# Kernel optimization log

Measured on AMD Instinct MI355X. Metric: run time of the kernel, lower is better.

Reference implementation:

```python
import jax, jax.numpy as jnp
import numpy as np

NUM_FEAT = 512
NUM_HEAD = 8
DEPTH = NUM_FEAT // NUM_HEAD
B, S = 2, 4096


def setup_inputs() -> dict:
    key = jax.random.key(0)
    ks = jax.random.split(key, 12)
    sc = 1.0 / np.sqrt(NUM_FEAT)
    inp = {
        "q": jax.random.normal(ks[0], (B, S, NUM_FEAT), jnp.float32),
        "k": jax.random.normal(ks[1], (B, S, NUM_FEAT), jnp.float32),
        "v": jax.random.normal(ks[2], (B, S, NUM_FEAT), jnp.float32),
        # causal mask: 1 where attention is disallowed (upper triangle), additive style
        "mask": jnp.triu(jnp.ones((S, S), jnp.float32), k=1)[None, None, :, :],
        "wq": jax.random.normal(ks[3], (NUM_FEAT, NUM_FEAT), jnp.float32) * sc,
        "bq": jnp.zeros((NUM_FEAT,), jnp.float32),
        "wk": jax.random.normal(ks[4], (NUM_FEAT, NUM_FEAT), jnp.float32) * sc,
        "bk": jnp.zeros((NUM_FEAT,), jnp.float32),
        "wv": jax.random.normal(ks[5], (NUM_FEAT, NUM_FEAT), jnp.float32) * sc,
        "bv": jnp.zeros((NUM_FEAT,), jnp.float32),
        "wo": jax.random.normal(ks[6], (NUM_FEAT, NUM_FEAT), jnp.float32) * sc,
        "bo": jnp.zeros((NUM_FEAT,), jnp.float32),
    }
    return inp


def _split_heads(x):
    b, s, _ = x.shape
    return x.reshape(b, s, NUM_HEAD, DEPTH).transpose(0, 2, 1, 3)  # [B,H,S,D]


def reference(q, k, v, mask, wq, bq, wk, bk, wv, bv, wo, bo):
    qh = _split_heads(q @ wq + bq)
    kh = _split_heads(k @ wk + bk)
    vh = _split_heads(v @ wv + bv)
    # scaled dot-product attention with materialized [B,H,S,S] scores
    logits = jnp.einsum("bhqd,bhkd->bhqk", qh, kh) / jnp.sqrt(jnp.float32(DEPTH))
    logits = logits + mask * (-1e9)
    weights = jax.nn.softmax(logits, axis=-1)
    attn = jnp.einsum("bhqk,bhkd->bhqd", weights, vh)
    concat = attn.transpose(0, 2, 1, 3).reshape(q.shape[0], -1, NUM_FEAT)
    return concat @ wo + bo
```

## Files before the change

### kernel.cpp

```cpp
#include <hip/hip_runtime.h>
#include <hip/hip_bf16.h>
#include <stdint.h>

#define NB 2
#define NS 4096
#define NF 512
#define NH 8
#define ND 64
#define NM (NB * NS)

typedef __attribute__((ext_vector_type(8))) short bf16x8;
typedef __attribute__((ext_vector_type(4))) float f32x4;
typedef __attribute__((ext_vector_type(16))) float f32x16;

static __device__ __forceinline__ unsigned short f2bf(float f) {
    union { float f; uint32_t u; } x; x.f = f;
    uint32_t u = x.u;
    u += 0x7FFFu + ((u >> 16) & 1u);
    return (unsigned short)(u >> 16);
}

static __device__ __forceinline__ void load_lds16(const void* g, void* l) {
    __builtin_amdgcn_global_load_lds(
        (const __attribute__((address_space(1))) void*)g,
        (__attribute__((address_space(3))) void*)l,
        16, 0, 0);
}

__global__ void convert_all(const float* __restrict__ q, const float* __restrict__ k,
                            const float* __restrict__ v,
                            unsigned short* __restrict__ qb, unsigned short* __restrict__ kb,
                            unsigned short* __restrict__ vb,
                            const float* __restrict__ wq, const float* __restrict__ wk,
                            const float* __restrict__ wv, const float* __restrict__ wo,
                            unsigned short* __restrict__ o0, unsigned short* __restrict__ o1,
                            unsigned short* __restrict__ o2, unsigned short* __restrict__ o3) {
    int i0 = blockIdx.x * blockDim.x + threadIdx.x;
    int stride = gridDim.x * blockDim.x;
    const int n4 = (NB * NS * NF) / 4;
    for (int i = i0; i < n4; i += stride) {
        float4 a = ((const float4*)q)[i];
        float4 b = ((const float4*)k)[i];
        float4 c = ((const float4*)v)[i];
        ushort4 oa, ob, oc;
        oa.x = f2bf(a.x); oa.y = f2bf(a.y); oa.z = f2bf(a.z); oa.w = f2bf(a.w);
        ob.x = f2bf(b.x); ob.y = f2bf(b.y); ob.z = f2bf(b.z); ob.w = f2bf(b.w);
        oc.x = f2bf(c.x); oc.y = f2bf(c.y); oc.z = f2bf(c.z); oc.w = f2bf(c.w);
        ((ushort4*)qb)[i] = oa;
        ((ushort4*)kb)[i] = ob;
        ((ushort4*)vb)[i] = oc;
    }
    for (int i = i0; i < 4 * NF * NF; i += stride) {
        int w = i >> 18;
        int off = i & (NF * NF - 1);
        int r = off >> 9;
        int c = off & (NF - 1);
        const float* src = (w == 0) ? wq : (w == 1) ? wk : (w == 2) ? wv : wo;
        unsigned short* dst = (w == 0) ? o0 : (w == 1) ? o1 : (w == 2) ? o2 : o3;
        dst[c * NF + r] = f2bf(src[off]);
    }
}

__launch_bounds__(256, 2)
__global__ void proj_qkv(const unsigned short* __restrict__ Aq,
                         const unsigned short* __restrict__ Ak,
                         const unsigned short* __restrict__ Av,
                         const unsigned short* __restrict__ WqT,
                         const unsigned short* __restrict__ WkT,
                         const unsigned short* __restrict__ WvT,
                         const float* __restrict__ bq, const float* __restrict__ bk,
                         const float* __restrict__ bv,
                         unsigned short* __restrict__ Qh, unsigned short* __restrict__ Kh,
                         unsigned short* __restrict__ VTs) {
    __shared__ char smem[65536];

    const int mode = blockIdx.z;
    const unsigned short* A  = (mode == 0) ? Aq : (mode == 1) ? Ak : Av;
    const unsigned short* WT = (mode == 0) ? WqT : (mode == 1) ? WkT : WvT;
    const float* bias        = (mode == 0) ? bq : (mode == 1) ? bk : bv;

    const int t = threadIdx.x;
    const int wid = t >> 6;
    const int lane = t & 63;
    const int l15 = lane & 15;
    const int lhi = lane >> 4;
    const int m0 = blockIdx.x * 128;
    const int n0 = blockIdx.y * 128;
    const int wm = (wid >> 1) * 64;
    const int wn = (wid & 1) * 64;

    const int srow = t >> 3;
    const int scol = ((t & 7) * 16) ^ ((srow & 7) << 4);

    const f32x4 zero4 = {0.f, 0.f, 0.f, 0.f};
    f32x4 acc[4][4];
#pragma unroll
    for (int i = 0; i < 4; ++i)
#pragma unroll
        for (int j = 0; j < 4; ++j) acc[i][j] = zero4;

    auto STAGE = [&](int buf, int k0) {
        char* As = smem + buf * 32768;
        char* Bs = As + 16384;
#pragma unroll
        for (int i = 0; i < 4; ++i) {
            const char* sa = (const char*)A + ((size_t)(m0 + i * 32 + srow) * NF + k0) * 2 + scol;
            load_lds16(sa, As + i * 4096 + wid * 1024);
            const char* sb = (const char*)WT + ((size_t)(n0 + i * 32 + srow) * NF + k0) * 2 + scol;
            load_lds16(sb, Bs + i * 4096 + wid * 1024);
        }
    };

    STAGE(0, 0);
    int cur = 0;
    for (int kt = 0; kt < 8; ++kt) {
        if (kt < 7) {
            STAGE(cur ^ 1, (kt + 1) * 64);
            asm volatile("s_waitcnt vmcnt(8)" ::: "memory");
        } else {
            asm volatile("s_waitcnt vmcnt(0)" ::: "memory");
        }
        __builtin_amdgcn_s_barrier();
        __builtin_amdgcn_sched_barrier(0);

        const char* As = smem + cur * 32768;
        const char* Bs = As + 16384;
#pragma unroll
        for (int ks = 0; ks < 2; ++ks) {
            bf16x8 af[4], bfr[4];
#pragma unroll
            for (int i = 0; i < 4; ++i) {
                int ra = wm + i * 16 + l15;
                int ca = (ks * 64 + lhi * 16) ^ ((ra & 7) << 4);
                af[i] = *(const bf16x8*)(As + ra * 128 + ca);
                int rb = wn + i * 16 + l15;
                int cb = (ks * 64 + lhi * 16) ^ ((rb & 7) << 4);
                bfr[i] = *(const bf16x8*)(Bs + rb * 128 + cb);
            }
#pragma unroll
            for (int mi = 0; mi < 4; ++mi)
#pragma unroll
                for (int ni = 0; ni < 4; ++ni)
                    acc[mi][ni] = __builtin_amdgcn_mfma_f32_16x16x32_bf16(af[mi], bfr[ni], acc[mi][ni], 0, 0, 0);
        }
        __builtin_amdgcn_sched_barrier(0);
        __builtin_amdgcn_s_barrier();
        cur ^= 1;
    }

#pragma unroll
    for (int ni = 0; ni < 4; ++ni) {
        int col = n0 + wn + ni * 16 + l15;
        float bv2 = bias[col];
#pragma unroll
        for (int mi = 0; mi < 4; ++mi) {
#pragma unroll
            for (int r = 0; r < 4; ++r) {
                int row = m0 + wm + mi * 16 + lhi * 4 + r;
                float val = acc[mi][ni][r] + bv2;
                int b = row >> 12, s = row & (NS - 1);
                int hh = col >> 6, d = col & (ND - 1);
                if (mode == 0) {
                    val *= 0.125f;
                    Qh[((size_t)(b * NH + hh) * NS + s) * ND + d] = f2bf(val);
                } else if (mode == 1) {
                    Kh[((size_t)(b * NH + hh) * NS + s) * ND + d] = f2bf(val);
                } else {
                    VTs[((size_t)(b * NH + hh) * ND + d) * NS + s] = f2bf(val);
                }
            }
        }
    }
}

__launch_bounds__(256, 2)
__global__ void proj_o(const unsigned short* __restrict__ A,
                       const unsigned short* __restrict__ WT,
                       const float* __restrict__ bias,
                       float* __restrict__ Out) {
    __shared__ char smem[49152];

    const int t = threadIdx.x;
    const int wid = t >> 6;
    const int lane = t & 63;
    const int l15 = lane & 15;
    const int lhi = lane >> 4;
    const int m0 = blockIdx.x * 64;
    const int n0 = blockIdx.y * 128;
    const int wm = (wid >> 1) * 32;
    const int wn = (wid & 1) * 64;

    const int srow = t >> 3;
    const int scol = ((t & 7) * 16) ^ ((srow & 7) << 4);

    const f32x4 zero4 = {0.f, 0.f, 0.f, 0.f};
    f32x4 acc[2][4];
#pragma unroll
    for (int i = 0; i < 2; ++i)
#pragma unroll
        for (int j = 0; j < 4; ++j) acc[i][j] = zero4;

    auto STAGE = [&](int buf, int k0) {
        char* As = smem + buf * 24576;
        char* Bs = As + 8192;
#pragma unroll
        for (int i = 0; i < 2; ++i) {
            const char* sa = (const char*)A + ((size_t)(m0 + i * 32 + srow) * NF + k0) * 2 + scol;
            load_lds16(sa, As + i * 4096 + wid * 1024);
        }
#pragma unroll
        for (int i = 0; i < 4; ++i) {
            const char* sb = (const char*)WT + ((size_t)(n0 + i * 32 + srow) * NF + k0) * 2 + scol;
            load_lds16(sb, Bs + i * 4096 + wid * 1024);
        }
    };

    STAGE(0, 0);
    int cur = 0;
    for (int kt = 0; kt < 8; ++kt) {
        if (kt < 7) {
            STAGE(cur ^ 1, (kt + 1) * 64);
            asm volatile("s_waitcnt vmcnt(6)" ::: "memory");
        } else {
            asm volatile("s_waitcnt vmcnt(0)" ::: "memory");
        }
        __builtin_amdgcn_s_barrier();
        __builtin_amdgcn_sched_barrier(0);

        const char* As = smem + cur * 24576;
        const char* Bs = As + 8192;
#pragma unroll
        for (int ks = 0; ks < 2; ++ks) {
            bf16x8 af[2], bfr[4];
#pragma unroll
            for (int i = 0; i < 2; ++i) {
                int ra = wm + i * 16 + l15;
                int ca = (ks * 64 + lhi * 16) ^ ((ra & 7) << 4);
                af[i] = *(const bf16x8*)(As + ra * 128 + ca);
            }
#pragma unroll
            for (int i = 0; i < 4; ++i) {
                int rb = wn + i * 16 + l15;
                int cb = (ks * 64 + lhi * 16) ^ ((rb & 7) << 4);
                bfr[i] = *(const bf16x8*)(Bs + rb * 128 + cb);
            }
#pragma unroll
            for (int mi = 0; mi < 2; ++mi)
#pragma unroll
                for (int ni = 0; ni < 4; ++ni)
                    acc[mi][ni] = __builtin_amdgcn_mfma_f32_16x16x32_bf16(af[mi], bfr[ni], acc[mi][ni], 0, 0, 0);
        }
        __builtin_amdgcn_sched_barrier(0);
        __builtin_amdgcn_s_barrier();
        cur ^= 1;
    }

#pragma unroll
    for (int ni = 0; ni < 4; ++ni) {
        int col = n0 + wn + ni * 16 + l15;
        float bv2 = bias[col];
#pragma unroll
        for (int mi = 0; mi < 2; ++mi)
#pragma unroll
            for (int r = 0; r < 4; ++r) {
                int row = m0 + wm + mi * 16 + lhi * 4 + r;
                Out[(size_t)row * NF + col] = acc[mi][ni][r] + bv2;
            }
    }
}

__launch_bounds__(256, 2)
__global__ void attn_fused(const unsigned short* __restrict__ Qh,
                           const unsigned short* __restrict__ Kh,
                           const unsigned short* __restrict__ VT,
                           unsigned short* __restrict__ Cc) {
    __shared__ char smem[65536];

    const int t = threadIdx.x;
    const int wid = t >> 6;
    const int pair = wid >> 1;
    const int a = wid & 1;
    const int lane = t & 63;
    const int l31 = lane & 31;
    const int h = lane >> 5;
    const int qt = 63 - (int)blockIdx.x;
    const int hh = blockIdx.y, b = blockIdx.z;
    const int q0 = qt * 64;
    const size_t bh = (size_t)b * NH + hh;
    const char* Qp = (const char*)(Qh + bh * NS * ND);
    const char* Kp = (const char*)(Kh + bh * NS * ND);
    const char* Vp = (const char*)(VT + bh * (size_t)ND * NS);

    const int qrow = q0 + a * 32 + l31;
    bf16x8 qf[4];
#pragma unroll
    for (int kc = 0; kc < 4; ++kc)
        qf[kc] = *(const bf16x8*)(Qp + (size_t)qrow * 128 + kc * 32 + h * 16);

    f32x16 o[2];
#pragma unroll
    for (int r = 0; r < 16; ++r) { o[0][r] = 0.f; o[1][r] = 0.f; }
    float m_run = -1e30f, l_run = 0.f;

    const int srow = lane >> 3;
    const int scol = ((lane & 7) * 16) ^ ((srow & 7) << 4);
    const size_t koff = (size_t)srow * 128 + scol;
    const size_t voff = (size_t)srow * (NS * 2) + scol;
    char* pbase = smem + pair * 32768;

    auto STAGE = [&](int buf, int kv0) {
        char* dst = pbase + buf * 16384;
        if (a == 0) {
            const char* g = Kp + (size_t)kv0 * 128 + koff;
#pragma unroll
            for (int i = 0; i < 8; ++i)
                load_lds16(g + i * 1024, dst + i * 1024);
        } else {
            const char* g = Vp + (size_t)kv0 * 2 + voff;
            char* lv = dst + 8192;
#pragma unroll
            for (int i = 0; i < 8; ++i)
                load_lds16(g + (size_t)i * 8 * (NS * 2), lv + i * 1024);
        }
    };

    const int myC = (qt + 2 - pair) >> 1;
    const int R = (qt + 2) >> 1;
    const int sw = (l31 & 7) << 4;

    if (0 < myC) STAGE(0, pair * 64);
    int cur = 0;

    for (int j = 0; j < R; ++j) {
        if (j + 1 < myC) {
            STAGE(cur ^ 1, (2 * (j + 1) + pair) * 64);
            asm volatile("s_waitcnt vmcnt(8)" ::: "memory");
        } else {
            asm volatile("s_waitcnt vmcnt(0)" ::: "memory");
        }
        __builtin_amdgcn_s_barrier();
        __builtin_amdgcn_sched_barrier(0);

        if (j < myC) {
            const int kt = 2 * j + pair;
            const char* Kb = pbase + cur * 16384;
            const char* Vb = Kb + 8192;

            f32x16 sT[2];
#pragma unroll
            for (int r = 0; r < 16; ++r) { sT[0][r] = 0.f; sT[1][r] = 0.f; }
#pragma unroll
            for (int kvi = 0; kvi < 2; ++kvi) {
                const int row = kvi * 32 + l31;
#pragma unroll
                for (int kc = 0; kc < 4; ++kc) {
                    bf16x8 kf = *(const bf16x8*)(Kb + row * 128 + ((kc * 32 + h * 16) ^ sw));
                    sT[kvi] = __builtin_amdgcn_mfma_f32_32x32x16_bf16(kf, qf[kc], sT[kvi], 0, 0, 0);
                }
            }

            if (kt == qt) {
#pragma unroll
                for (int kvi = 0; kvi < 2; ++kvi)
#pragma unroll
                    for (int r = 0; r < 16; ++r) {
                        int kv = kt * 64 + kvi * 32 + (r & 3) + ((r >> 2) << 3) + h * 4;
                        if (kv > qrow) sT[kvi][r] = -1e30f;
                    }
            }

            float pm = -1e30f;
#pragma unroll
            for (int kvi = 0; kvi < 2; ++kvi)
#pragma unroll
                for (int r = 0; r < 16; ++r) pm = fmaxf(pm, sT[kvi][r]);
            pm = fmaxf(pm, __shfl_xor(pm, 32));

            if (__ballot(pm > m_run + 8.0f) != 0ull) {
                float mnew = fmaxf(m_run, pm);
                float sc = __expf(m_run - mnew);
                m_run = mnew;
                l_run *= sc;
#pragma unroll
                for (int di = 0; di < 2; ++di)
#pragma unroll
                    for (int r = 0; r < 16; ++r) o[di][r] *= sc;
            }
            float rs = 0.f;
#pragma unroll
            for (int kvi = 0; kvi < 2; ++kvi)
#pragma unroll
                for (int r = 0; r < 16; ++r) {
                    float p = __expf(sT[kvi][r] - m_run);
                    sT[kvi][r] = p;
                    rs += p;
                }
            rs += __shfl_xor(rs, 32);
            l_run += rs;

            unsigned int w[2][8];
#pragma unroll
            for (int kvi = 0; kvi < 2; ++kvi)
#pragma unroll
                for (int i = 0; i < 8; ++i)
                    w[kvi][i] = (unsigned int)f2bf(sT[kvi][2 * i]) |
                                ((unsigned int)f2bf(sT[kvi][2 * i + 1]) << 16);

            union FB { unsigned int u[4]; bf16x8 v; };
            bf16x8 pf[4];
#pragma unroll
            for (int ck = 0; ck < 4; ++ck) {
                const int kvi = ck >> 1, pb = (ck & 1) * 4;
                unsigned int aSrc = h ? w[kvi][pb + 0] : w[kvi][pb + 2];
                unsigned int bSrc = h ? w[kvi][pb + 1] : w[kvi][pb + 3];
                unsigned int sA = (unsigned int)__shfl_xor((int)aSrc, 32);
                unsigned int sB = (unsigned int)__shfl_xor((int)bSrc, 32);
                FB f;
                f.u[0] = (h == 0) ? w[kvi][pb + 0] : sA;
                f.u[1] = (h == 0) ? w[kvi][pb + 1] : sB;
                f.u[2] = (h == 0) ? sA : w[kvi][pb + 2];
                f.u[3] = (h == 0) ? sB : w[kvi][pb + 3];
                pf[ck] = f.v;
            }

#pragma unroll
            for (int di = 0; di < 2; ++di) {
                const int row = di * 32 + l31;
#pragma unroll
                for (int ck = 0; ck < 4; ++ck) {
                    bf16x8 vf = *(const bf16x8*)(Vb + row * 128 + ((ck * 32 + h * 16) ^ sw));
                    o[di] = __builtin_amdgcn_mfma_f32_32x32x16_bf16(vf, pf[ck], o[di], 0, 0, 0);
                }
            }
        }

        __builtin_amdgcn_sched_barrier(0);
        __builtin_amdgcn_s_barrier();
        cur ^= 1;
    }

    __syncthreads();
    float* xch = (float*)smem;
    const int xi = (a * 64 + lane) * 34;
    if (pair == 1) {
        xch[xi] = m_run;
        xch[xi + 1] = l_run;
#pragma unroll
        for (int di = 0; di < 2; ++di)
#pragma unroll
            for (int r = 0; r < 16; ++r) xch[xi + 2 + di * 16 + r] = o[di][r];
    }
    __syncthreads();
    if (pair == 0) {
        float m1 = xch[xi], l1 = xch[xi + 1];
        float m = fmaxf(m_run, m1);
        float e0 = __expf(m_run - m);
        float e1 = __expf(m1 - m);
        float inv = 1.f / (l_run * e0 + l1 * e1);
        size_t obase = ((size_t)b * NS + qrow) * NF + hh * ND;
#pragma unroll
        for (int di = 0; di < 2; ++di)
#pragma unroll
            for (int tq = 0; tq < 4; ++tq) {
                ushort4 pk;
                pk.x = f2bf((o[di][4 * tq + 0] * e0 + xch[xi + 2 + di * 16 + 4 * tq + 0] * e1) * inv);
                pk.y = f2bf((o[di][4 * tq + 1] * e0 + xch[xi + 2 + di * 16 + 4 * tq + 1] * e1) * inv);
                pk.z = f2bf((o[di][4 * tq + 2] * e0 + xch[xi + 2 + di * 16 + 4 * tq + 2] * e1) * inv);
                pk.w = f2bf((o[di][4 * tq + 3] * e0 + xch[xi + 2 + di * 16 + 4 * tq + 3] * e1) * inv);
                *(ushort4*)(Cc + obase + di * 32 + tq * 8 + h * 4) = pk;
            }
    }
}

extern "C" void kernel_launch(void* const* d_in, const int* in_sizes, int n_in,
                              void* d_out, int out_size, void* d_ws, size_t ws_size,
                              hipStream_t stream) {
    const float* q = (const float*)d_in[0];
    const float* k = (const float*)d_in[1];
    const float* v = (const float*)d_in[2];
    const float* wq = (const float*)d_in[4];
    const float* bq = (const float*)d_in[5];
    const float* wk = (const float*)d_in[6];
    const float* bk = (const float*)d_in[7];
    const float* wv = (const float*)d_in[8];
    const float* bv = (const float*)d_in[9];
    const float* wo = (const float*)d_in[10];
    const float* bo = (const float*)d_in[11];

    const size_t MB = 1u << 20;
    char* ws = (char*)d_ws;
    unsigned short* qb  = (unsigned short*)(ws);
    unsigned short* kb  = (unsigned short*)(ws + 8 * MB);
    unsigned short* vb  = (unsigned short*)(ws + 16 * MB);
    unsigned short* wqT = (unsigned short*)(ws + 24 * MB);
    unsigned short* wkT = (unsigned short*)(ws + 24 * MB + 512 * 1024);
    unsigned short* wvT = (unsigned short*)(ws + 25 * MB);
    unsigned short* woT = (unsigned short*)(ws + 25 * MB + 512 * 1024);
    unsigned short* Qh  = (unsigned short*)(ws + 26 * MB);
    unsigned short* Kh  = (unsigned short*)(ws + 34 * MB);
    unsigned short* VTs = (unsigned short*)(ws + 42 * MB);

    convert_all<<<dim3(2048), dim3(256), 0, stream>>>(q, k, v, qb, kb, vb,
                                                      wq, wk, wv, wo, wqT, wkT, wvT, woT);

    proj_qkv<<<dim3(NM / 128, NF / 128, 3), dim3(256), 0, stream>>>(
        qb, kb, vb, wqT, wkT, wvT, bq, bk, bv, Qh, Kh, VTs);

    attn_fused<<<dim3(64, NH, NB), dim3(256), 0, stream>>>(Qh, Kh, VTs, qb );

    proj_o<<<dim3(NM / 64, NF / 128), dim3(256), 0, stream>>>(qb, woT, bo, (float*)d_out);
}
```

Baseline: 319.3 us.

## Restructure attention to single-wave blocks loading K/V directly into registers

Replaces the 4-wave block, which split the KV range between two wave pairs sharing LDS double buffers and then merged their softmax states, with one 64-thread block per 32-query tile. Each wave now walks the full causal KV range and ping-pongs K fragments in registers, loading them straight from global memory with no LDS, barriers or cross-pair merge. The grid grows to 2048 single-wave blocks ordered longest-first. This removes LDS staging and sync overhead but gives up K/V reuse across waves, so every wave reads K and V from global or cache on its own and register pressure rises.

```diff
diff --git a/kernel.cpp b/kernel.cpp
--- a/kernel.cpp
+++ b/kernel.cpp
@@ -269,29 +269,24 @@
     }
 }
 
-__launch_bounds__(256, 2)
+__launch_bounds__(64, 2)
 __global__ void attn_fused(const unsigned short* __restrict__ Qh,
                            const unsigned short* __restrict__ Kh,
                            const unsigned short* __restrict__ VT,
                            unsigned short* __restrict__ Cc) {
-    __shared__ char smem[65536];
-
-    const int t = threadIdx.x;
-    const int wid = t >> 6;
-    const int pair = wid >> 1;
-    const int a = wid & 1;
-    const int lane = t & 63;
+    const int lane = threadIdx.x;
     const int l31 = lane & 31;
     const int h = lane >> 5;
-    const int qt = 63 - (int)blockIdx.x;
-    const int hh = blockIdx.y, b = blockIdx.z;
-    const int q0 = qt * 64;
-    const size_t bh = (size_t)b * NH + hh;
-    const char* Qp = (const char*)(Qh + bh * NS * ND);
-    const char* Kp = (const char*)(Kh + bh * NS * ND);
-    const char* Vp = (const char*)(VT + bh * (size_t)ND * NS);
-
-    const int qrow = q0 + a * 32 + l31;
+    const int k = blockIdx.x;
+    const int bh = k & 15;
+    const int g = 127 - (k >> 4);
+    const int b = bh >> 3, hh = bh & 7;
+    const size_t bhs = (size_t)b * NH + hh;
+    const char* Qp = (const char*)(Qh + bhs * NS * ND);
+    const char* Kp = (const char*)(Kh + bhs * NS * ND);
+    const char* Vp = (const char*)(VT + bhs * (size_t)ND * NS);
+
+    const int qrow = g * 32 + l31;
     bf16x8 qf[4];
 #pragma unroll
     for (int kc = 0; kc < 4; ++kc)
@@ -302,174 +297,133 @@
     for (int r = 0; r < 16; ++r) { o[0][r] = 0.f; o[1][r] = 0.f; }
     float m_run = -1e30f, l_run = 0.f;
 
-    const int srow = lane >> 3;
-    const int scol = ((lane & 7) * 16) ^ ((srow & 7) << 4);
-    const size_t koff = (size_t)srow * 128 + scol;
-    const size_t voff = (size_t)srow * (NS * 2) + scol;
-    char* pbase = smem + pair * 32768;
-
-    auto STAGE = [&](int buf, int kv0) {
-        char* dst = pbase + buf * 16384;
-        if (a == 0) {
-            const char* g = Kp + (size_t)kv0 * 128 + koff;
+    const int nkv = (g >> 1) + 1;
+
+    auto LOADK = [&](int t, bf16x8* kf) {
+        const char* base = Kp + (size_t)t * 64 * 128;
+#pragma unroll
+        for (int kvi = 0; kvi < 2; ++kvi)
+#pragma unroll
+            for (int kc = 0; kc < 4; ++kc)
+                kf[kvi * 4 + kc] = *(const bf16x8*)(base + (kvi * 32 + l31) * 128 + kc * 32 + h * 16);
+    };
+    auto LOADV = [&](int t, bf16x8* vf) {
+        const char* base = Vp + (size_t)t * 128;
+#pragma unroll
+        for (int di = 0; di < 2; ++di)
+#pragma unroll
+            for (int ck = 0; ck < 4; ++ck)
+                vf[di * 4 + ck] = *(const bf16x8*)(base + (size_t)(di * 32 + l31) * (NS * 2) + ck * 32 + h * 16);
+    };
+
+    auto TILE = [&](int t, const bf16x8* kf, const bf16x8* vf) {
+        f32x16 sT[2];
+#pragma unroll
+        for (int r = 0; r < 16; ++r) { sT[0][r] = 0.f; sT[1][r] = 0.f; }
+#pragma unroll
+        for (int kvi = 0; kvi < 2; ++kvi)
+#pragma unroll
+            for (int kc = 0; kc < 4; ++kc)
+                sT[kvi] = __builtin_amdgcn_mfma_f32_32x32x16_bf16(kf[kvi * 4 + kc], qf[kc], sT[kvi], 0, 0, 0);
+
+        if (t == nkv - 1) {
+#pragma unroll
+            for (int kvi = 0; kvi < 2; ++kvi)
+#pragma unroll
+                for (int r = 0; r < 16; ++r) {
+                    int kv = t * 64 + kvi * 32 + (r & 3) + ((r >> 2) << 3) + h * 4;
+                    if (kv > qrow) sT[kvi][r] = -1e30f;
+                }
+        }
+
+        float pm = -1e30f;
+#pragma unroll
+        for (int kvi = 0; kvi < 2; ++kvi)
+#pragma unroll
+            for (int r = 0; r < 16; ++r) pm = fmaxf(pm, sT[kvi][r]);
+        pm = fmaxf(pm, __shfl_xor(pm, 32));
+
+        if (__ballot(pm > m_run + 8.0f) != 0ull) {
+            float mnew = fmaxf(m_run, pm);
+            float sc = __expf(m_run - mnew);
+            m_run = mnew;
+            l_run *= sc;
+#pragma unroll
+            for (int di = 0; di < 2; ++di)
+#pragma unroll
+                for (int r = 0; r < 16; ++r) o[di][r] *= sc;
+        }
+        float rs = 0.f;
+#pragma unroll
+        for (int kvi = 0; kvi < 2; ++kvi)
+#pragma unroll
+            for (int r = 0; r < 16; ++r) {
+                float p = __expf(sT[kvi][r] - m_run);
+                sT[kvi][r] = p;
+                rs += p;
+            }
+        rs += __shfl_xor(rs, 32);
+        l_run += rs;
+
+        unsigned int w[2][8];
+#pragma unroll
+        for (int kvi = 0; kvi < 2; ++kvi)
 #pragma unroll
             for (int i = 0; i < 8; ++i)
-                load_lds16(g + i * 1024, dst + i * 1024);
-        } else {
-            const char* g = Vp + (size_t)kv0 * 2 + voff;
-            char* lv = dst + 8192;
-#pragma unroll
-            for (int i = 0; i < 8; ++i)
-                load_lds16(g + (size_t)i * 8 * (NS * 2), lv + i * 1024);
-        }
+                w[kvi][i] = (unsigned int)f2bf(sT[kvi][2 * i]) |
+                            ((unsigned int)f2bf(sT[kvi][2 * i + 1]) << 16);
+
+        union FB { unsigned int u[4]; bf16x8 v; };
+        bf16x8 pf[4];
+#pragma unroll
+        for (int ck = 0; ck < 4; ++ck) {
+            const int kvi = ck >> 1, pb = (ck & 1) * 4;
+            unsigned int aSrc = h ? w[kvi][pb + 0] : w[kvi][pb + 2];
+            unsigned int bSrc = h ? w[kvi][pb + 1] : w[kvi][pb + 3];
+            unsigned int sA = (unsigned int)__shfl_xor((int)aSrc, 32);
+            unsigned int sB = (unsigned int)__shfl_xor((int)bSrc, 32);
+            FB f;
+            f.u[0] = (h == 0) ? w[kvi][pb + 0] : sA;
+            f.u[1] = (h == 0) ? w[kvi][pb + 1] : sB;
+            f.u[2] = (h == 0) ? sA : w[kvi][pb + 2];
+            f.u[3] = (h == 0) ? sB : w[kvi][pb + 3];
+            pf[ck] = f.v;
+        }
+
+#pragma unroll
+        for (int di = 0; di < 2; ++di)
+#pragma unroll
+            for (int ck = 0; ck < 4; ++ck)
+                o[di] = __builtin_amdgcn_mfma_f32_32x32x16_bf16(vf[di * 4 + ck], pf[ck], o[di], 0, 0, 0);
     };
 
-    const int myC = (qt + 2 - pair) >> 1;
-    const int R = (qt + 2) >> 1;
-    const int sw = (l31 & 7) << 4;
-
-    if (0 < myC) STAGE(0, pair * 64);
-    int cur = 0;
-
-    for (int j = 0; j < R; ++j) {
-        if (j + 1 < myC) {
-            STAGE(cur ^ 1, (2 * (j + 1) + pair) * 64);
-            asm volatile("s_waitcnt vmcnt(8)" ::: "memory");
-        } else {
-            asm volatile("s_waitcnt vmcnt(0)" ::: "memory");
-        }
-        __builtin_amdgcn_s_barrier();
-        __builtin_amdgcn_sched_barrier(0);
-
-        if (j < myC) {
-            const int kt = 2 * j + pair;
-            const char* Kb = pbase + cur * 16384;
-            const char* Vb = Kb + 8192;
-
-            f32x16 sT[2];
-#pragma unroll
-            for (int r = 0; r < 16; ++r) { sT[0][r] = 0.f; sT[1][r] = 0.f; }
-#pragma unroll
-            for (int kvi = 0; kvi < 2; ++kvi) {
-                const int row = kvi * 32 + l31;
-#pragma unroll
-                for (int kc = 0; kc < 4; ++kc) {
-                    bf16x8 kf = *(const bf16x8*)(Kb + row * 128 + ((kc * 32 + h * 16) ^ sw));
-                    sT[kvi] = __builtin_amdgcn_mfma_f32_32x32x16_bf16(kf, qf[kc], sT[kvi], 0, 0, 0);
-                }
-            }
-
-            if (kt == qt) {
-#pragma unroll
-                for (int kvi = 0; kvi < 2; ++kvi)
-#pragma unroll
-                    for (int r = 0; r < 16; ++r) {
-                        int kv = kt * 64 + kvi * 32 + (r & 3) + ((r >> 2) << 3) + h * 4;
-                        if (kv > qrow) sT[kvi][r] = -1e30f;
-                    }
-            }
-
-            float pm = -1e30f;
-#pragma unroll
-            for (int kvi = 0; kvi < 2; ++kvi)
-#pragma unroll
-                for (int r = 0; r < 16; ++r) pm = fmaxf(pm, sT[kvi][r]);
-            pm = fmaxf(pm, __shfl_xor(pm, 32));
-
-            if (__ballot(pm > m_run + 8.0f) != 0ull) {
-                float mnew = fmaxf(m_run, pm);
-                float sc = __expf(m_run - mnew);
-                m_run = mnew;
-                l_run *= sc;
-#pragma unroll
-                for (int di = 0; di < 2; ++di)
-#pragma unroll
-                    for (int r = 0; r < 16; ++r) o[di][r] *= sc;
-            }
-            float rs = 0.f;
-#pragma unroll
-            for (int kvi = 0; kvi < 2; ++kvi)
-#pragma unroll
-                for (int r = 0; r < 16; ++r) {
-                    float p = __expf(sT[kvi][r] - m_run);
-                    sT[kvi][r] = p;
-                    rs += p;
-                }
-            rs += __shfl_xor(rs, 32);
-            l_run += rs;
-
-            unsigned int w[2][8];
-#pragma unroll
-            for (int kvi = 0; kvi < 2; ++kvi)
-#pragma unroll
-                for (int i = 0; i < 8; ++i)
-                    w[kvi][i] = (unsigned int)f2bf(sT[kvi][2 * i]) |
-                                ((unsigned int)f2bf(sT[kvi][2 * i + 1]) << 16);
-
-            union FB { unsigned int u[4]; bf16x8 v; };
-            bf16x8 pf[4];
-#pragma unroll
-            for (int ck = 0; ck < 4; ++ck) {
-                const int kvi = ck >> 1, pb = (ck & 1) * 4;
-                unsigned int aSrc = h ? w[kvi][pb + 0] : w[kvi][pb + 2];
-                unsigned int bSrc = h ? w[kvi][pb + 1] : w[kvi][pb + 3];
-                unsigned int sA = (unsigned int)__shfl_xor((int)aSrc, 32);
-                unsigned int sB = (unsigned int)__shfl_xor((int)bSrc, 32);
-                FB f;
-                f.u[0] = (h == 0) ? w[kvi][pb + 0] : sA;
-                f.u[1] = (h == 0) ? w[kvi][pb + 1] : sB;
-                f.u[2] = (h == 0) ? sA : w[kvi][pb + 2];
-                f.u[3] = (h == 0) ? sB : w[kvi][pb + 3];
-                pf[ck] = f.v;
-            }
-
-#pragma unroll
-            for (int di = 0; di < 2; ++di) {
-                const int row = di * 32 + l31;
-#pragma unroll
-                for (int ck = 0; ck < 4; ++ck) {
-                    bf16x8 vf = *(const bf16x8*)(Vb + row * 128 + ((ck * 32 + h * 16) ^ sw));
-                    o[di] = __builtin_amdgcn_mfma_f32_32x32x16_bf16(vf, pf[ck], o[di], 0, 0, 0);
-                }
-            }
-        }
-
-        __builtin_amdgcn_sched_barrier(0);
-        __builtin_amdgcn_s_barrier();
-        cur ^= 1;
-    }
-
-    __syncthreads();
-    float* xch = (float*)smem;
-    const int xi = (a * 64 + lane) * 34;
-    if (pair == 1) {
-        xch[xi] = m_run;
-        xch[xi + 1] = l_run;
-#pragma unroll
-        for (int di = 0; di < 2; ++di)
-#pragma unroll
-            for (int r = 0; r < 16; ++r) xch[xi + 2 + di * 16 + r] = o[di][r];
-    }
-    __syncthreads();
-    if (pair == 0) {
-        float m1 = xch[xi], l1 = xch[xi + 1];
-        float m = fmaxf(m_run, m1);
-        float e0 = __expf(m_run - m);
-        float e1 = __expf(m1 - m);
-        float inv = 1.f / (l_run * e0 + l1 * e1);
-        size_t obase = ((size_t)b * NS + qrow) * NF + hh * ND;
-#pragma unroll
-        for (int di = 0; di < 2; ++di)
-#pragma unroll
-            for (int tq = 0; tq < 4; ++tq) {
-                ushort4 pk;
-                pk.x = f2bf((o[di][4 * tq + 0] * e0 + xch[xi + 2 + di * 16 + 4 * tq + 0] * e1) * inv);
-                pk.y = f2bf((o[di][4 * tq + 1] * e0 + xch[xi + 2 + di * 16 + 4 * tq + 1] * e1) * inv);
-                pk.z = f2bf((o[di][4 * tq + 2] * e0 + xch[xi + 2 + di * 16 + 4 * tq + 2] * e1) * inv);
-                pk.w = f2bf((o[di][4 * tq + 3] * e0 + xch[xi + 2 + di * 16 + 4 * tq + 3] * e1) * inv);
-                *(ushort4*)(Cc + obase + di * 32 + tq * 8 + h * 4) = pk;
-            }
-    }
+    bf16x8 kA[8], kB[8], vv[8];
+    LOADK(0, kA);
+    int t = 0;
+    while (true) {
+        LOADV(t, vv);
+        if (t + 1 < nkv) LOADK(t + 1, kB);
+        TILE(t, kA, vv);
+        if (++t >= nkv) break;
+        LOADV(t, vv);
+        if (t + 1 < nkv) LOADK(t + 1, kA);
+        TILE(t, kB, vv);
+        if (++t >= nkv) break;
+    }
+
+    float inv = 1.0f / l_run;
+    size_t obase = ((size_t)b * NS + qrow) * NF + hh * ND;
+#pragma unroll
+    for (int di = 0; di < 2; ++di)
+#pragma unroll
+        for (int tq = 0; tq < 4; ++tq) {
+            ushort4 pk;
+            pk.x = f2bf(o[di][4 * tq + 0] * inv);
+            pk.y = f2bf(o[di][4 * tq + 1] * inv);
+            pk.z = f2bf(o[di][4 * tq + 2] * inv);
+            pk.w = f2bf(o[di][4 * tq + 3] * inv);
+            *(ushort4*)(Cc + obase + di * 32 + tq * 8 + h * 4) = pk;
+        }
 }
 
 extern "C" void kernel_launch(void* const* d_in, const int* in_sizes, int n_in,
@@ -506,7 +460,7 @@
     proj_qkv<<<dim3(NM / 128, NF / 128, 3), dim3(256), 0, stream>>>(
         qb, kb, vb, wqT, wkT, wvT, bq, bk, bv, Qh, Kh, VTs);
 
-    attn_fused<<<dim3(64, NH, NB), dim3(256), 0, stream>>>(Qh, Kh, VTs, qb );
+    attn_fused<<<dim3(2048), dim3(64), 0, stream>>>(Qh, Kh, VTs, qb );
 
     proj_o<<<dim3(NM / 64, NF / 128), dim3(256), 0, stream>>>(qb, woT, bo, (float*)d_out);
 }
```

After: 334.3 us. 1.05x slower.
